# Kernel tuning notes

Hardware: AMD Instinct MI355X
Metric: run time of the kernel (lower is better)

## Reference

```python
import jax, jax.numpy as jnp
import numpy as np

B, N, F_IN, F_OUT = 8, 2048, 256, 256
NEG_SLOPE = 0.2
EPS = 1e-7


def setup_inputs() -> dict:
    key = jax.random.key(0)
    k1, k2, k3, k4, k5 = jax.random.split(key, 5)
    x = jax.random.normal(k1, (B, N, F_IN), dtype=jnp.float32)
    # A is a 0/1 adjacency mask used as float in the module
    A = jax.random.bernoulli(k2, 0.5, (B, N, N)).astype(jnp.float32)
    # W: xavier_normal_ init, shape [in_features, out_features]
    W = jax.random.normal(k3, (F_IN, F_OUT), dtype=jnp.float32) * np.sqrt(2.0 / (F_IN + F_OUT))
    # attention_mechanism: Linear(2*F_OUT, 1) -> weight vector [2*F_OUT], scalar bias
    bound = 1.0 / np.sqrt(2 * F_OUT)
    a_w = jax.random.uniform(k4, (2 * F_OUT,), dtype=jnp.float32, minval=-bound, maxval=bound)
    a_b = jax.random.uniform(k5, (), dtype=jnp.float32, minval=-bound, maxval=bound)
    return {"A": A, "x": x, "W": W, "a_w": a_w, "a_b": a_b}


def reference(A, x, W, a_w, a_b):
    # Wh = x @ W : [B, N, F_OUT]
    Wh = jnp.einsum('bnf,fo->bno', x, W)
    # Linear([Wh_i ; Wh_j]) == Wh_i @ a_w[:F] + Wh_j @ a_w[F:] + b  (no O(N^2 F) concat)
    s_src = Wh @ a_w[:F_OUT]   # [B, N] contribution of row index i
    s_dst = Wh @ a_w[F_OUT:]   # [B, N] contribution of col index j
    e = s_src[:, :, None] + s_dst[:, None, :] + a_b  # [B, N, N]
    e = jnp.where(e > 0, e, NEG_SLOPE * e)           # leaky_relu(0.2)
    # masked softmax over dim=1 (as in the original module)
    exps = jnp.exp(e) * A
    sums = jnp.sum(exps, axis=1, keepdims=True) + EPS
    attn = exps / sums                                # [B, N, N]
    return jnp.einsum('bij,bjo->bio', attn, Wh)       # [B, N, F_OUT]
```

## Files before the change

kernel.cpp:

```cpp
#include <hip/hip_runtime.h>
#include <hip/hip_bf16.h>

#define NN 2048
#define BB 8
#define FD 256
#define NEG_SLOPE 0.2f
#define EPSV 1e-7f

typedef __bf16 bf16x8 __attribute__((ext_vector_type(8)));
typedef __bf16 bf16x4 __attribute__((ext_vector_type(4)));
typedef float f32x4 __attribute__((ext_vector_type(4)));

__device__ __forceinline__ void gload16(const __bf16* g, __bf16* l) {
    __builtin_amdgcn_global_load_lds((const __attribute__((address_space(1))) unsigned int*)g,
                                     (__attribute__((address_space(3))) unsigned int*)l,
                                     16, 0, 0);
}

__global__ __launch_bounds__(256) void k1_prep(const float* __restrict__ W,
                                               __bf16* __restrict__ WT) {
    int idx = blockIdx.x * 256 + threadIdx.x;
    int o = idx >> 8, f = idx & 255;
    WT[idx] = (__bf16)W[f * FD + o];
}

__global__ __launch_bounds__(256) void k2_whgemm(const float* __restrict__ x,
                                                 const __bf16* __restrict__ WT,
                                                 const float* __restrict__ a_w,
                                                 float* __restrict__ Wh,
                                                 float* __restrict__ s_src,
                                                 float* __restrict__ s_dst) {
    const int wave = threadIdx.x >> 6;
    const int lane = threadIdx.x & 63;
    const int row0 = blockIdx.x * 32 + (wave >> 1) * 16;
    const int ohalf = (wave & 1) * 128;
    const int m = lane & 15;
    const int quad = lane >> 4;
    const int row = row0 + m;
    const float* xrow = x + (size_t)row * FD + quad * 8;

    f32x4 acc[8];
#pragma unroll
    for (int n = 0; n < 8; ++n) acc[n] = (f32x4){0.f, 0.f, 0.f, 0.f};

    for (int k0 = 0; k0 < FD; k0 += 32) {
        float4 xa = *(const float4*)(xrow + k0);
        float4 xb = *(const float4*)(xrow + k0 + 4);
        bf16x8 af;
        af[0] = (__bf16)xa.x; af[1] = (__bf16)xa.y; af[2] = (__bf16)xa.z; af[3] = (__bf16)xa.w;
        af[4] = (__bf16)xb.x; af[5] = (__bf16)xb.y; af[6] = (__bf16)xb.z; af[7] = (__bf16)xb.w;
#pragma unroll
        for (int n = 0; n < 8; ++n) {
            int o = ohalf + n * 16 + m;
            bf16x8 bf = *(const bf16x8*)(WT + o * FD + k0 + quad * 8);
            acc[n] = __builtin_amdgcn_mfma_f32_16x16x32_bf16(af, bf, acc[n], 0, 0, 0);
        }
    }
#pragma unroll
    for (int n = 0; n < 8; ++n) {
        int o = ohalf + n * 16 + m;
#pragma unroll
        for (int r = 0; r < 4; ++r) {
            Wh[(size_t)(row0 + quad * 4 + r) * FD + o] = acc[n][r];
        }
    }

    float psrc[4] = {0.f, 0.f, 0.f, 0.f};
    float pdst[4] = {0.f, 0.f, 0.f, 0.f};
#pragma unroll
    for (int n = 0; n < 8; ++n) {
        int o = ohalf + n * 16 + m;
        float awS = a_w[o], awD = a_w[FD + o];
#pragma unroll
        for (int r = 0; r < 4; ++r) {
            psrc[r] += acc[n][r] * awS;
            pdst[r] += acc[n][r] * awD;
        }
    }
#pragma unroll
    for (int off = 1; off <= 8; off <<= 1) {
#pragma unroll
        for (int r = 0; r < 4; ++r) {
            psrc[r] += __shfl_xor(psrc[r], off, 64);
            pdst[r] += __shfl_xor(pdst[r], off, 64);
        }
    }
    __shared__ float sS[2][2][16], sD[2][2][16];
    if (m == 0) {
        int rp = wave >> 1, oh = wave & 1;
#pragma unroll
        for (int r = 0; r < 4; ++r) {
            sS[rp][oh][quad * 4 + r] = psrc[r];
            sD[rp][oh][quad * 4 + r] = pdst[r];
        }
    }
    __syncthreads();
    if (threadIdx.x < 32) {
        int rp = threadIdx.x >> 4, idx = threadIdx.x & 15;
        int orow = blockIdx.x * 32 + rp * 16 + idx;
        s_src[orow] = sS[rp][0][idx] + sS[rp][1][idx];
        s_dst[orow] = sD[rp][0][idx] + sD[rp][1][idx];
    }
}

__global__ __launch_bounds__(256) void k4_den(const float* __restrict__ A,
                                              const float* __restrict__ s_src,
                                              const float* __restrict__ s_dst,
                                              const float* __restrict__ a_bp,
                                              float* __restrict__ den_part) {
    const int blk = blockIdx.x;
    const int b = blk & 7;
    const int jhalf = (blk >> 3) & 1;
    const int isp = blk >> 4;
    const int i0 = isp * 32;
    const int j = jhalf * 1024 + threadIdx.x * 4;
    __shared__ float ss[32];
    if (threadIdx.x < 32) ss[threadIdx.x] = s_src[b * NN + i0 + threadIdx.x] + a_bp[0];
    __syncthreads();
    float4 sd = *(const float4*)(s_dst + b * NN + j);
    float ax = 0.f, ay = 0.f, az = 0.f, aw = 0.f;
    const float* Ap = A + ((size_t)b * NN + i0) * NN + j;
#pragma unroll 8
    for (int i = 0; i < 32; ++i) {
        float4 a = *(const float4*)(Ap + (size_t)i * NN);
        float si = ss[i];
        float e0 = si + sd.x; e0 = e0 > 0.f ? e0 : NEG_SLOPE * e0;
        float e1 = si + sd.y; e1 = e1 > 0.f ? e1 : NEG_SLOPE * e1;
        float e2 = si + sd.z; e2 = e2 > 0.f ? e2 : NEG_SLOPE * e2;
        float e3 = si + sd.w; e3 = e3 > 0.f ? e3 : NEG_SLOPE * e3;
        ax += a.x * __expf(e0);
        ay += a.y * __expf(e1);
        az += a.z * __expf(e2);
        aw += a.w * __expf(e3);
    }
    float4 r = (float4){ax, ay, az, aw};
    *(float4*)(den_part + (size_t)isp * (BB * NN) + b * NN + j) = r;
}

__global__ __launch_bounds__(256) void k5_wht(const float* __restrict__ Wh,
                                              const float* __restrict__ den_part,
                                              __bf16* __restrict__ WhT) {
    const int b = blockIdx.z;
    const int j0 = blockIdx.x * 64;
    const int o0 = blockIdx.y * 64;
    __shared__ float tile[64][65];
    __shared__ float invd[64];
    if (threadIdx.x < 64) {
        float s = 0.f;
        const float* dp = den_part + b * NN + j0 + threadIdx.x;
#pragma unroll 8
        for (int sI = 0; sI < 64; ++sI) s += dp[(size_t)sI * (BB * NN)];
        invd[threadIdx.x] = 1.f / (s + EPSV);
    }
    __syncthreads();
    int jr = threadIdx.x >> 4, oc = (threadIdx.x & 15) * 4;
#pragma unroll
    for (int p = 0; p < 4; ++p) {
        int jj = jr + p * 16;
        float4 v = *(const float4*)(Wh + (size_t)(b * NN + j0 + jj) * FD + o0 + oc);
        float s = invd[jj];
        tile[jj][oc + 0] = v.x * s;
        tile[jj][oc + 1] = v.y * s;
        tile[jj][oc + 2] = v.z * s;
        tile[jj][oc + 3] = v.w * s;
    }
    __syncthreads();
    int ow = threadIdx.x >> 4, jc = (threadIdx.x & 15) * 4;
#pragma unroll
    for (int p = 0; p < 4; ++p) {
        int o = ow + p * 16;
        bf16x4 wv;
        wv[0] = (__bf16)tile[jc + 0][o];
        wv[1] = (__bf16)tile[jc + 1][o];
        wv[2] = (__bf16)tile[jc + 2][o];
        wv[3] = (__bf16)tile[jc + 3][o];
        *(bf16x4*)(WhT + (size_t)(b * FD + o0 + o) * NN + j0 + jc) = wv;
    }
}

__global__ __launch_bounds__(256) void k6f(const float* __restrict__ A,
                                           const __bf16* __restrict__ WhT,
                                           const float* __restrict__ s_src,
                                           const float* __restrict__ s_dst,
                                           const float* __restrict__ a_bp,
                                           float* __restrict__ out) {
    __shared__ __bf16 lP[2][64 * 64];
    __shared__ __bf16 lB[2][128 * 64];
    const int blk = blockIdx.x;
    const int b = blk & 7;
    const int r_ = blk >> 3;
    const int nh = r_ & 1;
    const int mt = r_ >> 1;
    const int i0 = mt * 64;
    const int o0 = nh * 128;
    const int t = threadIdx.x;
    const int w = t >> 6, lane = t & 63;
    const int m = lane & 15, quad = lane >> 4;
    const int wr = w >> 1, wc = w & 1;

    const int srow = lane >> 3;
    const int schunk = (lane & 7) ^ srow;
    const __bf16* gB = WhT + ((size_t)(b * FD + o0 + w * 8 + srow)) * NN + schunk * 8;

#define STAGEB(buf, step) { \
        const __bf16* gb = gB + (step) * 64; \
        gload16(gb,                   &lB[buf][0] + (w * 8) * 64); \
        gload16(gb + (size_t)32 * NN, &lB[buf][0] + (32 + w * 8) * 64); \
        gload16(gb + (size_t)64 * NN, &lB[buf][0] + (64 + w * 8) * 64); \
        gload16(gb + (size_t)96 * NN, &lB[buf][0] + (96 + w * 8) * 64); \
    }

    const int pr = t >> 2;
    const int pc = (t & 3) * 16;
    const float ssr = s_src[b * NN + i0 + pr] + a_bp[0];
    const float* Ap  = A + ((size_t)(b * NN + i0 + pr)) * NN + pc;
    const float* sdp = s_dst + b * NN + pc;
    const int ch0 = pc >> 3;
    const int sw0 = ((ch0    ) ^ (pr & 7)) * 8;
    const int sw1 = ((ch0 + 1) ^ (pr & 7)) * 8;
    __bf16* lProw = &lP[0][0] + pr * 64;

    float4 a0E, a1E, a2E, a3E, d0E, d1E, d2E, d3E;
    float4 a0O, a1O, a2O, a3O, d0O, d1O, d2O, d3O;
#define LOADP(step, S) { \
        const float* ap = Ap  + (step) * 64; \
        const float* dp = sdp + (step) * 64; \
        a0##S = *(const float4*)(ap + 0);  a1##S = *(const float4*)(ap + 4); \
        a2##S = *(const float4*)(ap + 8);  a3##S = *(const float4*)(ap + 12); \
        d0##S = *(const float4*)(dp + 0);  d1##S = *(const float4*)(dp + 4); \
        d2##S = *(const float4*)(dp + 8);  d3##S = *(const float4*)(dp + 12); \
    }
#define PB1(vv, idx, av, dv) { \
        float e = ssr + dv; e = e > 0.f ? e : NEG_SLOPE * e; \
        vv[idx] = (__bf16)(av * __expf(e)); }
#define PBUILD(buf, S) { \
        bf16x8 v0, v1; \
        PB1(v0, 0, a0##S.x, d0##S.x) PB1(v0, 1, a0##S.y, d0##S.y) \
        PB1(v0, 2, a0##S.z, d0##S.z) PB1(v0, 3, a0##S.w, d0##S.w) \
        PB1(v0, 4, a1##S.x, d1##S.x) PB1(v0, 5, a1##S.y, d1##S.y) \
        PB1(v0, 6, a1##S.z, d1##S.z) PB1(v0, 7, a1##S.w, d1##S.w) \
        PB1(v1, 0, a2##S.x, d2##S.x) PB1(v1, 1, a2##S.y, d2##S.y) \
        PB1(v1, 2, a2##S.z, d2##S.z) PB1(v1, 3, a2##S.w, d2##S.w) \
        PB1(v1, 4, a3##S.x, d3##S.x) PB1(v1, 5, a3##S.y, d3##S.y) \
        PB1(v1, 6, a3##S.z, d3##S.z) PB1(v1, 7, a3##S.w, d3##S.w) \
        *(bf16x8*)(lProw + (buf) * 4096 + sw0) = v0; \
        *(bf16x8*)(lProw + (buf) * 4096 + sw1) = v1; \
    }

#define MFMA_BLOCK(cur) { \
        const __bf16* lPc = &lP[cur][0]; \
        const __bf16* lBc = &lB[cur][0]; \
        _Pragma("unroll") \
        for (int ks = 0; ks < 2; ++ks) { \
            const int kof = (ks * 32 + quad * 8) ^ swz; \
            bf16x8 pa0 = *(const bf16x8*)(lPc + (wr * 32 + m) * 64 + kof); \
            bf16x8 pa1 = *(const bf16x8*)(lPc + (wr * 32 + 16 + m) * 64 + kof); \
            _Pragma("unroll") \
            for (int n = 0; n < 4; ++n) { \
                bf16x8 bfr = *(const bf16x8*)(lBc + (wc * 64 + n * 16 + m) * 64 + kof); \
                acc[0][n] = __builtin_amdgcn_mfma_f32_16x16x32_bf16(pa0, bfr, acc[0][n], 0, 0, 0); \
                acc[1][n] = __builtin_amdgcn_mfma_f32_16x16x32_bf16(pa1, bfr, acc[1][n], 0, 0, 0); \
            } \
        } \
    }

    LOADP(0, E)
    STAGEB(0, 0)
    PBUILD(0, E)
    LOADP(1, O)

    f32x4 acc[2][4];
#pragma unroll
    for (int mi = 0; mi < 2; ++mi)
#pragma unroll
        for (int n = 0; n < 4; ++n) acc[mi][n] = (f32x4){0.f, 0.f, 0.f, 0.f};

    const int swz = (m & 7) * 8;
    for (int kt2 = 0; kt2 < 16; ++kt2) {
        const int kt = kt2 * 2;
        __syncthreads();
        if (kt2 < 15) LOADP(kt + 2, E)
        STAGEB(1, kt + 1)
        MFMA_BLOCK(0)
        PBUILD(1, O)
        __syncthreads();
        if (kt2 < 15) {
            LOADP(kt + 3, O)
            STAGEB(0, kt + 2)
        }
        MFMA_BLOCK(1)
        if (kt2 < 15) PBUILD(0, E)
    }

#pragma unroll
    for (int mi = 0; mi < 2; ++mi)
#pragma unroll
        for (int n = 0; n < 4; ++n) {
            int o = o0 + wc * 64 + n * 16 + m;
#pragma unroll
            for (int rr = 0; rr < 4; ++rr) {
                int orow = i0 + wr * 32 + mi * 16 + quad * 4 + rr;
                out[((size_t)b * NN + orow) * FD + o] = acc[mi][n][rr];
            }
        }
#undef STAGEB
#undef LOADP
#undef PB1
#undef PBUILD
#undef MFMA_BLOCK
}

extern "C" void kernel_launch(void* const* d_in, const int* in_sizes, int n_in,
                              void* d_out, int out_size, void* d_ws, size_t ws_size,
                              hipStream_t stream) {
    const float* A   = (const float*)d_in[0];
    const float* x   = (const float*)d_in[1];
    const float* W   = (const float*)d_in[2];
    const float* a_w = (const float*)d_in[3];
    const float* a_b = (const float*)d_in[4];
    float* out = (float*)d_out;

    char* ws = (char*)d_ws;
    __bf16* WT      = (__bf16*)ws;
    float*  Wh      = (float*)(ws + 131072);
    __bf16* WhT     = (__bf16*)(ws + 16908288);
    float*  s_src   = (float*)(ws + 25296896);
    float*  s_dst   = (float*)(ws + 25362432);
    float*  den_part= (float*)(ws + 25427968);

    k1_prep<<<256, 256, 0, stream>>>(W, WT);
    k2_whgemm<<<512, 256, 0, stream>>>(x, WT, a_w, Wh, s_src, s_dst);
    k4_den<<<1024, 256, 0, stream>>>(A, s_src, s_dst, a_b, den_part);
    k5_wht<<<dim3(32, 4, 8), 256, 0, stream>>>(Wh, den_part, WhT);
    k6f<<<512, 256, 0, stream>>>(A, WhT, s_src, s_dst, a_b, out);
}
```

Measured before the change: 292.6 us.

## Compute attention scores via W·a_w and fuse Wh GEMM into scaled transpose

Scores s_src/s_dst are now computed as x·(W·a_w) in a small fp32 kernel, with no dependence on Wh. The W transpose is merged into the same launch. The Wh GEMM moves after the denominator kernel and writes the denominator-scaled bf16 transposed WhT directly through LDS. This removes the fp32 Wh round-trip through global memory and one kernel launch. The scores now come from fp32 math rather than the bf16 GEMM output, which slightly changes numerics, and the tileT LDS buffer (~33KB) may limit occupancy.

```diff
diff --git a/kernel.cpp b/kernel.cpp
--- a/kernel.cpp
+++ b/kernel.cpp
@@ -17,90 +17,48 @@
                                      16, 0, 0);
 }
 
-__global__ __launch_bounds__(256) void k1_prep(const float* __restrict__ W,
-                                               __bf16* __restrict__ WT) {
-    int idx = blockIdx.x * 256 + threadIdx.x;
-    int o = idx >> 8, f = idx & 255;
-    WT[idx] = (__bf16)W[f * FD + o];
-}
-
-__global__ __launch_bounds__(256) void k2_whgemm(const float* __restrict__ x,
-                                                 const __bf16* __restrict__ WT,
-                                                 const float* __restrict__ a_w,
-                                                 float* __restrict__ Wh,
-                                                 float* __restrict__ s_src,
-                                                 float* __restrict__ s_dst) {
-    const int wave = threadIdx.x >> 6;
-    const int lane = threadIdx.x & 63;
-    const int row0 = blockIdx.x * 32 + (wave >> 1) * 16;
-    const int ohalf = (wave & 1) * 128;
-    const int m = lane & 15;
-    const int quad = lane >> 4;
-    const int row = row0 + m;
-    const float* xrow = x + (size_t)row * FD + quad * 8;
-
-    f32x4 acc[8];
-#pragma unroll
-    for (int n = 0; n < 8; ++n) acc[n] = (f32x4){0.f, 0.f, 0.f, 0.f};
-
-    for (int k0 = 0; k0 < FD; k0 += 32) {
-        float4 xa = *(const float4*)(xrow + k0);
-        float4 xb = *(const float4*)(xrow + k0 + 4);
-        bf16x8 af;
-        af[0] = (__bf16)xa.x; af[1] = (__bf16)xa.y; af[2] = (__bf16)xa.z; af[3] = (__bf16)xa.w;
-        af[4] = (__bf16)xb.x; af[5] = (__bf16)xb.y; af[6] = (__bf16)xb.z; af[7] = (__bf16)xb.w;
-#pragma unroll
-        for (int n = 0; n < 8; ++n) {
-            int o = ohalf + n * 16 + m;
-            bf16x8 bf = *(const bf16x8*)(WT + o * FD + k0 + quad * 8);
-            acc[n] = __builtin_amdgcn_mfma_f32_16x16x32_bf16(af, bf, acc[n], 0, 0, 0);
+__global__ __launch_bounds__(256) void k1s(const float* __restrict__ W,
+                                           const float* __restrict__ a_w,
+                                           const float* __restrict__ x,
+                                           __bf16* __restrict__ WT,
+                                           float* __restrict__ s_src,
+                                           float* __restrict__ s_dst) {
+    const int bid = blockIdx.x, tid = threadIdx.x;
+    if (bid >= 64) {
+        int idx = (bid - 64) * 256 + tid;
+        int o = idx >> 8, f = idx & 255;
+        WT[idx] = (__bf16)W[f * FD + o];
+        return;
+    }
+    __shared__ float aw[2 * FD];
+    __shared__ float vs[FD], vd[FD];
+    aw[tid] = a_w[tid];
+    aw[FD + tid] = a_w[FD + tid];
+    __syncthreads();
+    {
+        const float* wrow = W + (size_t)tid * FD;
+        float s1 = 0.f, s2 = 0.f;
+#pragma unroll 8
+        for (int k = 0; k < FD; k += 4) {
+            float4 wv = *(const float4*)(wrow + k);
+            s1 += wv.x * aw[k] + wv.y * aw[k + 1] + wv.z * aw[k + 2] + wv.w * aw[k + 3];
+            s2 += wv.x * aw[FD + k] + wv.y * aw[FD + k + 1]
+                + wv.z * aw[FD + k + 2] + wv.w * aw[FD + k + 3];
         }
-    }
-#pragma unroll
-    for (int n = 0; n < 8; ++n) {
-        int o = ohalf + n * 16 + m;
-#pragma unroll
-        for (int r = 0; r < 4; ++r) {
-            Wh[(size_t)(row0 + quad * 4 + r) * FD + o] = acc[n][r];
-        }
-    }
-
-    float psrc[4] = {0.f, 0.f, 0.f, 0.f};
-    float pdst[4] = {0.f, 0.f, 0.f, 0.f};
-#pragma unroll
-    for (int n = 0; n < 8; ++n) {
-        int o = ohalf + n * 16 + m;
-        float awS = a_w[o], awD = a_w[FD + o];
-#pragma unroll
-        for (int r = 0; r < 4; ++r) {
-            psrc[r] += acc[n][r] * awS;
-            pdst[r] += acc[n][r] * awD;
-        }
-    }
-#pragma unroll
-    for (int off = 1; off <= 8; off <<= 1) {
-#pragma unroll
-        for (int r = 0; r < 4; ++r) {
-            psrc[r] += __shfl_xor(psrc[r], off, 64);
-            pdst[r] += __shfl_xor(pdst[r], off, 64);
-        }
-    }
-    __shared__ float sS[2][2][16], sD[2][2][16];
-    if (m == 0) {
-        int rp = wave >> 1, oh = wave & 1;
-#pragma unroll
-        for (int r = 0; r < 4; ++r) {
-            sS[rp][oh][quad * 4 + r] = psrc[r];
-            sD[rp][oh][quad * 4 + r] = pdst[r];
-        }
+        vs[tid] = s1; vd[tid] = s2;
     }
     __syncthreads();
-    if (threadIdx.x < 32) {
-        int rp = threadIdx.x >> 4, idx = threadIdx.x & 15;
-        int orow = blockIdx.x * 32 + rp * 16 + idx;
-        s_src[orow] = sS[rp][0][idx] + sS[rp][1][idx];
-        s_dst[orow] = sD[rp][0][idx] + sD[rp][1][idx];
-    }
+    const int row = bid * 256 + tid;
+    const float* xr = x + (size_t)row * FD;
+    float ss = 0.f, dd = 0.f;
+#pragma unroll 8
+    for (int k = 0; k < FD; k += 4) {
+        float4 xv = *(const float4*)(xr + k);
+        ss += xv.x * vs[k] + xv.y * vs[k + 1] + xv.z * vs[k + 2] + xv.w * vs[k + 3];
+        dd += xv.x * vd[k] + xv.y * vd[k + 1] + xv.z * vd[k + 2] + xv.w * vd[k + 3];
+    }
+    s_src[row] = ss;
+    s_dst[row] = dd;
 }
 
 __global__ __launch_bounds__(256) void k4_den(const float* __restrict__ A,
@@ -137,45 +95,74 @@
     *(float4*)(den_part + (size_t)isp * (BB * NN) + b * NN + j) = r;
 }
 
-__global__ __launch_bounds__(256) void k5_wht(const float* __restrict__ Wh,
-                                              const float* __restrict__ den_part,
-                                              __bf16* __restrict__ WhT) {
-    const int b = blockIdx.z;
-    const int j0 = blockIdx.x * 64;
-    const int o0 = blockIdx.y * 64;
-    __shared__ float tile[64][65];
-    __shared__ float invd[64];
-    if (threadIdx.x < 64) {
+__global__ __launch_bounds__(256) void k2n(const float* __restrict__ x,
+                                           const __bf16* __restrict__ WT,
+                                           const float* __restrict__ den_part,
+                                           __bf16* __restrict__ WhT) {
+    const int wave = threadIdx.x >> 6;
+    const int lane = threadIdx.x & 63;
+    const int gr0 = blockIdx.x * 32;
+    const int b = gr0 >> 11;
+    const int j0 = gr0 & (NN - 1);
+    const int row0 = gr0 + (wave >> 1) * 16;
+    const int ohalf = (wave & 1) * 128;
+    const int m = lane & 15;
+    const int quad = lane >> 4;
+    const float* xrow = x + (size_t)(row0 + m) * FD + quad * 8;
+
+    __shared__ float tileT[32][257];
+    __shared__ float invd[32];
+
+    if (threadIdx.x < 32) {
         float s = 0.f;
         const float* dp = den_part + b * NN + j0 + threadIdx.x;
 #pragma unroll 8
         for (int sI = 0; sI < 64; ++sI) s += dp[(size_t)sI * (BB * NN)];
         invd[threadIdx.x] = 1.f / (s + EPSV);
     }
+
+    f32x4 acc[8];
+#pragma unroll
+    for (int n = 0; n < 8; ++n) acc[n] = (f32x4){0.f, 0.f, 0.f, 0.f};
+
+    for (int k0 = 0; k0 < FD; k0 += 32) {
+        float4 xa = *(const float4*)(xrow + k0);
+        float4 xb = *(const float4*)(xrow + k0 + 4);
+        bf16x8 af;
+        af[0] = (__bf16)xa.x; af[1] = (__bf16)xa.y; af[2] = (__bf16)xa.z; af[3] = (__bf16)xa.w;
+        af[4] = (__bf16)xb.x; af[5] = (__bf16)xb.y; af[6] = (__bf16)xb.z; af[7] = (__bf16)xb.w;
+#pragma unroll
+        for (int n = 0; n < 8; ++n) {
+            int o = ohalf + n * 16 + m;
+            bf16x8 bf = *(const bf16x8*)(WT + o * FD + k0 + quad * 8);
+            acc[n] = __builtin_amdgcn_mfma_f32_16x16x32_bf16(af, bf, acc[n], 0, 0, 0);
+        }
+    }
+
+    const int jl = (wave >> 1) * 16 + quad * 4;
+#pragma unroll
+    for (int n = 0; n < 8; ++n) {
+        int o = ohalf + n * 16 + m;
+#pragma unroll
+        for (int r = 0; r < 4; ++r) tileT[jl + r][o] = acc[n][r];
+    }
     __syncthreads();
-    int jr = threadIdx.x >> 4, oc = (threadIdx.x & 15) * 4;
-#pragma unroll
-    for (int p = 0; p < 4; ++p) {
-        int jj = jr + p * 16;
-        float4 v = *(const float4*)(Wh + (size_t)(b * NN + j0 + jj) * FD + o0 + oc);
-        float s = invd[jj];
-        tile[jj][oc + 0] = v.x * s;
-        tile[jj][oc + 1] = v.y * s;
-        tile[jj][oc + 2] = v.z * s;
-        tile[jj][oc + 3] = v.w * s;
-    }
-    __syncthreads();
-    int ow = threadIdx.x >> 4, jc = (threadIdx.x & 15) * 4;
-#pragma unroll
-    for (int p = 0; p < 4; ++p) {
-        int o = ow + p * 16;
-        bf16x4 wv;
-        wv[0] = (__bf16)tile[jc + 0][o];
-        wv[1] = (__bf16)tile[jc + 1][o];
-        wv[2] = (__bf16)tile[jc + 2][o];
-        wv[3] = (__bf16)tile[jc + 3][o];
-        *(bf16x4*)(WhT + (size_t)(b * FD + o0 + o) * NN + j0 + jc) = wv;
-    }
+
+    const int o = threadIdx.x;
+    bf16x8 p0, p1, p2, p3;
+#pragma unroll
+    for (int jj = 0; jj < 8; ++jj)  p0[jj] = (__bf16)(tileT[jj][o] * invd[jj]);
+#pragma unroll
+    for (int jj = 0; jj < 8; ++jj)  p1[jj] = (__bf16)(tileT[8 + jj][o] * invd[8 + jj]);
+#pragma unroll
+    for (int jj = 0; jj < 8; ++jj)  p2[jj] = (__bf16)(tileT[16 + jj][o] * invd[16 + jj]);
+#pragma unroll
+    for (int jj = 0; jj < 8; ++jj)  p3[jj] = (__bf16)(tileT[24 + jj][o] * invd[24 + jj]);
+    __bf16* dst = WhT + (size_t)(b * FD + o) * NN + j0;
+    *(bf16x8*)(dst)      = p0;
+    *(bf16x8*)(dst + 8)  = p1;
+    *(bf16x8*)(dst + 16) = p2;
+    *(bf16x8*)(dst + 24) = p3;
 }
 
 __global__ __launch_bounds__(256) void k6f(const float* __restrict__ A,
@@ -322,15 +309,13 @@
 
     char* ws = (char*)d_ws;
     __bf16* WT      = (__bf16*)ws;
-    float*  Wh      = (float*)(ws + 131072);
-    __bf16* WhT     = (__bf16*)(ws + 16908288);
-    float*  s_src   = (float*)(ws + 25296896);
-    float*  s_dst   = (float*)(ws + 25362432);
-    float*  den_part= (float*)(ws + 25427968);
-
-    k1_prep<<<256, 256, 0, stream>>>(W, WT);
-    k2_whgemm<<<512, 256, 0, stream>>>(x, WT, a_w, Wh, s_src, s_dst);
+    __bf16* WhT     = (__bf16*)(ws + 131072);
+    float*  s_src   = (float*)(ws + 8519680);
+    float*  s_dst   = (float*)(ws + 8585216);
+    float*  den_part= (float*)(ws + 8650752);
+
+    k1s<<<320, 256, 0, stream>>>(W, a_w, x, WT, s_src, s_dst);
     k4_den<<<1024, 256, 0, stream>>>(A, s_src, s_dst, a_b, den_part);
-    k5_wht<<<dim3(32, 4, 8), 256, 0, stream>>>(Wh, den_part, WhT);
+    k2n<<<512, 256, 0, stream>>>(x, WT, den_part, WhT);
     k6f<<<512, 256, 0, stream>>>(A, WhT, s_src, s_dst, a_b, out);
 }
```

After: 300.4 us. 2.7% more time.

## Retile attention GEMM to full output width and load B fragments directly

Applied to the files above, without the earlier changes.

The fused attention-times-Wh kernel now assigns each block 32 rows and all 256 output columns instead of 64 rows by 128 columns. This removes the duplicated reading of the adjacency mask and the duplicated exp/leaky-relu construction of P across two column-half blocks. The WhT operand is loaded from global memory directly into registers per wave instead of being staged through LDS, which shrinks shared memory use. In exchange, the WhT read volume rises and the B loads go uncoalesced-ish per fragment, raising register pressure and latency exposure.

```diff
diff --git a/kernel.cpp b/kernel.cpp
--- a/kernel.cpp
+++ b/kernel.cpp
@@ -10,12 +10,6 @@
 typedef __bf16 bf16x8 __attribute__((ext_vector_type(8)));
 typedef __bf16 bf16x4 __attribute__((ext_vector_type(4)));
 typedef float f32x4 __attribute__((ext_vector_type(4)));
-
-__device__ __forceinline__ void gload16(const __bf16* g, __bf16* l) {
-    __builtin_amdgcn_global_load_lds((const __attribute__((address_space(1))) unsigned int*)g,
-                                     (__attribute__((address_space(3))) unsigned int*)l,
-                                     16, 0, 0);
-}
 
 __global__ __launch_bounds__(256) void k1_prep(const float* __restrict__ W,
                                                __bf16* __restrict__ WT) {
@@ -178,96 +172,102 @@
     }
 }
 
-__global__ __launch_bounds__(256) void k6f(const float* __restrict__ A,
-                                           const __bf16* __restrict__ WhT,
-                                           const float* __restrict__ s_src,
-                                           const float* __restrict__ s_dst,
-                                           const float* __restrict__ a_bp,
-                                           float* __restrict__ out) {
-    __shared__ __bf16 lP[2][64 * 64];
-    __shared__ __bf16 lB[2][128 * 64];
+__global__ __launch_bounds__(256) void k6f3(const float* __restrict__ A,
+                                            const __bf16* __restrict__ WhT,
+                                            const float* __restrict__ s_src,
+                                            const float* __restrict__ s_dst,
+                                            const float* __restrict__ a_bp,
+                                            float* __restrict__ out) {
+    __shared__ __bf16 lP[2][32 * 64];
     const int blk = blockIdx.x;
     const int b = blk & 7;
-    const int r_ = blk >> 3;
-    const int nh = r_ & 1;
-    const int mt = r_ >> 1;
-    const int i0 = mt * 64;
-    const int o0 = nh * 128;
+    const int mt = blk >> 3;
+    const int i0 = mt * 32;
     const int t = threadIdx.x;
     const int w = t >> 6, lane = t & 63;
     const int m = lane & 15, quad = lane >> 4;
-    const int wr = w >> 1, wc = w & 1;
-
-    const int srow = lane >> 3;
-    const int schunk = (lane & 7) ^ srow;
-    const __bf16* gB = WhT + ((size_t)(b * FD + o0 + w * 8 + srow)) * NN + schunk * 8;
-
-#define STAGEB(buf, step) { \
-        const __bf16* gb = gB + (step) * 64; \
-        gload16(gb,                   &lB[buf][0] + (w * 8) * 64); \
-        gload16(gb + (size_t)32 * NN, &lB[buf][0] + (32 + w * 8) * 64); \
-        gload16(gb + (size_t)64 * NN, &lB[buf][0] + (64 + w * 8) * 64); \
-        gload16(gb + (size_t)96 * NN, &lB[buf][0] + (96 + w * 8) * 64); \
-    }
-
-    const int pr = t >> 2;
-    const int pc = (t & 3) * 16;
+
+    const __bf16* gB0 = WhT + ((size_t)(b * FD + w * 64 +  0 + m)) * NN + quad * 8;
+    const __bf16* gB1 = WhT + ((size_t)(b * FD + w * 64 + 16 + m)) * NN + quad * 8;
+    const __bf16* gB2 = WhT + ((size_t)(b * FD + w * 64 + 32 + m)) * NN + quad * 8;
+    const __bf16* gB3 = WhT + ((size_t)(b * FD + w * 64 + 48 + m)) * NN + quad * 8;
+
+    bf16x8 b0aE, b1aE, b2aE, b3aE, b0bE, b1bE, b2bE, b3bE;
+    bf16x8 b0aO, b1aO, b2aO, b3aO, b0bO, b1bO, b2bO, b3bO;
+#define LOADB(step, S) { \
+        b0a##S = *(const bf16x8*)(gB0 + (size_t)(step) * 64); \
+        b1a##S = *(const bf16x8*)(gB1 + (size_t)(step) * 64); \
+        b2a##S = *(const bf16x8*)(gB2 + (size_t)(step) * 64); \
+        b3a##S = *(const bf16x8*)(gB3 + (size_t)(step) * 64); \
+        b0b##S = *(const bf16x8*)(gB0 + (size_t)(step) * 64 + 32); \
+        b1b##S = *(const bf16x8*)(gB1 + (size_t)(step) * 64 + 32); \
+        b2b##S = *(const bf16x8*)(gB2 + (size_t)(step) * 64 + 32); \
+        b3b##S = *(const bf16x8*)(gB3 + (size_t)(step) * 64 + 32); \
+    }
+
+    const int pr = t >> 3;
+    const int pc = (t & 7) * 8;
     const float ssr = s_src[b * NN + i0 + pr] + a_bp[0];
     const float* Ap  = A + ((size_t)(b * NN + i0 + pr)) * NN + pc;
     const float* sdp = s_dst + b * NN + pc;
-    const int ch0 = pc >> 3;
-    const int sw0 = ((ch0    ) ^ (pr & 7)) * 8;
-    const int sw1 = ((ch0 + 1) ^ (pr & 7)) * 8;
+    const int pdst = (((t & 7) ^ (pr & 7)) * 8);
     __bf16* lProw = &lP[0][0] + pr * 64;
 
-    float4 a0E, a1E, a2E, a3E, d0E, d1E, d2E, d3E;
-    float4 a0O, a1O, a2O, a3O, d0O, d1O, d2O, d3O;
+    float4 a0E, a1E, d0E, d1E, a0O, a1O, d0O, d1O;
 #define LOADP(step, S) { \
-        const float* ap = Ap  + (step) * 64; \
-        const float* dp = sdp + (step) * 64; \
-        a0##S = *(const float4*)(ap + 0);  a1##S = *(const float4*)(ap + 4); \
-        a2##S = *(const float4*)(ap + 8);  a3##S = *(const float4*)(ap + 12); \
-        d0##S = *(const float4*)(dp + 0);  d1##S = *(const float4*)(dp + 4); \
-        d2##S = *(const float4*)(dp + 8);  d3##S = *(const float4*)(dp + 12); \
-    }
-#define PB1(vv, idx, av, dv) { \
+        a0##S = *(const float4*)(Ap + (size_t)(step) * 64); \
+        a1##S = *(const float4*)(Ap + (size_t)(step) * 64 + 4); \
+        d0##S = *(const float4*)(sdp + (size_t)(step) * 64); \
+        d1##S = *(const float4*)(sdp + (size_t)(step) * 64 + 4); \
+    }
+#define PB1(pv, i, av, dv) { \
         float e = ssr + dv; e = e > 0.f ? e : NEG_SLOPE * e; \
-        vv[idx] = (__bf16)(av * __expf(e)); }
+        pv[i] = (__bf16)(av * __expf(e)); }
 #define PBUILD(buf, S) { \
-        bf16x8 v0, v1; \
-        PB1(v0, 0, a0##S.x, d0##S.x) PB1(v0, 1, a0##S.y, d0##S.y) \
-        PB1(v0, 2, a0##S.z, d0##S.z) PB1(v0, 3, a0##S.w, d0##S.w) \
-        PB1(v0, 4, a1##S.x, d1##S.x) PB1(v0, 5, a1##S.y, d1##S.y) \
-        PB1(v0, 6, a1##S.z, d1##S.z) PB1(v0, 7, a1##S.w, d1##S.w) \
-        PB1(v1, 0, a2##S.x, d2##S.x) PB1(v1, 1, a2##S.y, d2##S.y) \
-        PB1(v1, 2, a2##S.z, d2##S.z) PB1(v1, 3, a2##S.w, d2##S.w) \
-        PB1(v1, 4, a3##S.x, d3##S.x) PB1(v1, 5, a3##S.y, d3##S.y) \
-        PB1(v1, 6, a3##S.z, d3##S.z) PB1(v1, 7, a3##S.w, d3##S.w) \
-        *(bf16x8*)(lProw + (buf) * 4096 + sw0) = v0; \
-        *(bf16x8*)(lProw + (buf) * 4096 + sw1) = v1; \
-    }
-
-#define MFMA_BLOCK(cur) { \
+        bf16x8 pv; \
+        PB1(pv, 0, a0##S.x, d0##S.x) PB1(pv, 1, a0##S.y, d0##S.y) \
+        PB1(pv, 2, a0##S.z, d0##S.z) PB1(pv, 3, a0##S.w, d0##S.w) \
+        PB1(pv, 4, a1##S.x, d1##S.x) PB1(pv, 5, a1##S.y, d1##S.y) \
+        PB1(pv, 6, a1##S.z, d1##S.z) PB1(pv, 7, a1##S.w, d1##S.w) \
+        *(bf16x8*)(lProw + (buf) * 2048 + pdst) = pv; \
+    }
+
+    const int psw = m & 7;
+#define MFMA_BLOCK(cur, S) { \
         const __bf16* lPc = &lP[cur][0]; \
-        const __bf16* lBc = &lB[cur][0]; \
-        _Pragma("unroll") \
-        for (int ks = 0; ks < 2; ++ks) { \
-            const int kof = (ks * 32 + quad * 8) ^ swz; \
-            bf16x8 pa0 = *(const bf16x8*)(lPc + (wr * 32 + m) * 64 + kof); \
-            bf16x8 pa1 = *(const bf16x8*)(lPc + (wr * 32 + 16 + m) * 64 + kof); \
-            _Pragma("unroll") \
-            for (int n = 0; n < 4; ++n) { \
-                bf16x8 bfr = *(const bf16x8*)(lBc + (wc * 64 + n * 16 + m) * 64 + kof); \
-                acc[0][n] = __builtin_amdgcn_mfma_f32_16x16x32_bf16(pa0, bfr, acc[0][n], 0, 0, 0); \
-                acc[1][n] = __builtin_amdgcn_mfma_f32_16x16x32_bf16(pa1, bfr, acc[1][n], 0, 0, 0); \
-            } \
+        { \
+            const int kof = ((0 * 4 + quad) ^ psw) * 8; \
+            bf16x8 pa0 = *(const bf16x8*)(lPc + (m) * 64 + kof); \
+            bf16x8 pa1 = *(const bf16x8*)(lPc + (16 + m) * 64 + kof); \
+            acc[0][0] = __builtin_amdgcn_mfma_f32_16x16x32_bf16(pa0, b0a##S, acc[0][0], 0, 0, 0); \
+            acc[1][0] = __builtin_amdgcn_mfma_f32_16x16x32_bf16(pa1, b0a##S, acc[1][0], 0, 0, 0); \
+            acc[0][1] = __builtin_amdgcn_mfma_f32_16x16x32_bf16(pa0, b1a##S, acc[0][1], 0, 0, 0); \
+            acc[1][1] = __builtin_amdgcn_mfma_f32_16x16x32_bf16(pa1, b1a##S, acc[1][1], 0, 0, 0); \
+            acc[0][2] = __builtin_amdgcn_mfma_f32_16x16x32_bf16(pa0, b2a##S, acc[0][2], 0, 0, 0); \
+            acc[1][2] = __builtin_amdgcn_mfma_f32_16x16x32_bf16(pa1, b2a##S, acc[1][2], 0, 0, 0); \
+            acc[0][3] = __builtin_amdgcn_mfma_f32_16x16x32_bf16(pa0, b3a##S, acc[0][3], 0, 0, 0); \
+            acc[1][3] = __builtin_amdgcn_mfma_f32_16x16x32_bf16(pa1, b3a##S, acc[1][3], 0, 0, 0); \
         } \
+        { \
+            const int kof = ((1 * 4 + quad) ^ psw) * 8; \
+            bf16x8 pa0 = *(const bf16x8*)(lPc + (m) * 64 + kof); \
+            bf16x8 pa1 = *(const bf16x8*)(lPc + (16 + m) * 64 + kof); \
+            acc[0][0] = __builtin_amdgcn_mfma_f32_16x16x32_bf16(pa0, b0b##S, acc[0][0], 0, 0, 0); \
+            acc[1][0] = __builtin_amdgcn_mfma_f32_16x16x32_bf16(pa1, b0b##S, acc[1][0], 0, 0, 0); \
+            acc[0][1] = __builtin_amdgcn_mfma_f32_16x16x32_bf16(pa0, b1b##S, acc[0][1], 0, 0, 0); \
+            acc[1][1] = __builtin_amdgcn_mfma_f32_16x16x32_bf16(pa1, b1b##S, acc[1][1], 0, 0, 0); \
+            acc[0][2] = __builtin_amdgcn_mfma_f32_16x16x32_bf16(pa0, b2b##S, acc[0][2], 0, 0, 0); \
+            acc[1][2] = __builtin_amdgcn_mfma_f32_16x16x32_bf16(pa1, b2b##S, acc[1][2], 0, 0, 0); \
+            acc[0][3] = __builtin_amdgcn_mfma_f32_16x16x32_bf16(pa0, b3b##S, acc[0][3], 0, 0, 0); \
+            acc[1][3] = __builtin_amdgcn_mfma_f32_16x16x32_bf16(pa1, b3b##S, acc[1][3], 0, 0, 0); \
+        } \
     }
 
     LOADP(0, E)
-    STAGEB(0, 0)
     PBUILD(0, E)
     LOADP(1, O)
+    LOADB(0, E)
+    LOADB(1, O)
 
     f32x4 acc[2][4];
 #pragma unroll
@@ -275,35 +275,34 @@
 #pragma unroll
         for (int n = 0; n < 4; ++n) acc[mi][n] = (f32x4){0.f, 0.f, 0.f, 0.f};
 
-    const int swz = (m & 7) * 8;
     for (int kt2 = 0; kt2 < 16; ++kt2) {
         const int kt = kt2 * 2;
         __syncthreads();
         if (kt2 < 15) LOADP(kt + 2, E)
-        STAGEB(1, kt + 1)
-        MFMA_BLOCK(0)
+        MFMA_BLOCK(0, E)
+        if (kt2 < 15) LOADB(kt + 2, E)
         PBUILD(1, O)
         __syncthreads();
+        if (kt2 < 15) LOADP(kt + 3, O)
+        MFMA_BLOCK(1, O)
         if (kt2 < 15) {
-            LOADP(kt + 3, O)
-            STAGEB(0, kt + 2)
-        }
-        MFMA_BLOCK(1)
-        if (kt2 < 15) PBUILD(0, E)
+            LOADB(kt + 3, O)
+            PBUILD(0, E)
+        }
     }
 
 #pragma unroll
     for (int mi = 0; mi < 2; ++mi)
 #pragma unroll
         for (int n = 0; n < 4; ++n) {
-            int o = o0 + wc * 64 + n * 16 + m;
+            int o = w * 64 + n * 16 + m;
 #pragma unroll
             for (int rr = 0; rr < 4; ++rr) {
-                int orow = i0 + wr * 32 + mi * 16 + quad * 4 + rr;
+                int orow = i0 + mi * 16 + quad * 4 + rr;
                 out[((size_t)b * NN + orow) * FD + o] = acc[mi][n][rr];
             }
         }
-#undef STAGEB
+#undef LOADB
 #undef LOADP
 #undef PB1
 #undef PBUILD
@@ -332,5 +331,5 @@
     k2_whgemm<<<512, 256, 0, stream>>>(x, WT, a_w, Wh, s_src, s_dst);
     k4_den<<<1024, 256, 0, stream>>>(A, s_src, s_dst, a_b, den_part);
     k5_wht<<<dim3(32, 4, 8), 256, 0, stream>>>(Wh, den_part, WhT);
-    k6f<<<512, 256, 0, stream>>>(A, WhT, s_src, s_dst, a_b, out);
-}
+    k6f3<<<512, 256, 0, stream>>>(A, WhT, s_src, s_dst, a_b, out);
+}
```

New measurement: 305.2 us. 1.04x slower.
